# Performance work log

Hardware: AMD Instinct MI355X
Metric: run time of the kernel (lower is better)

Reference implementation:

```python
import jax, jax.numpy as jnp
import numpy as np

EPS = 1e-5
COMMITMENT_WEIGHT = 1.0


def setup_inputs() -> dict:
    key = jax.random.key(0)
    k1, k2 = jax.random.split(key)
    x = jax.random.normal(k1, (4, 4096, 128), dtype=jnp.float32)
    codebook = jax.random.normal(k2, (8192, 128), dtype=jnp.float32)
    return {"x": x, "codebook": codebook}


def _layernorm(x):
    # LayerNorm over last dim, elementwise_affine=False, eps=1e-5
    mu = jnp.mean(x, axis=-1, keepdims=True)
    var = jnp.mean(jnp.square(x - mu), axis=-1, keepdims=True)
    return (x - mu) * jax.lax.rsqrt(var + EPS)


def reference(x, codebook):
    b, n, d = x.shape
    xn = _layernorm(x)                      # [b, n, d]
    flat = xn.reshape(b * n, d)             # [bn, d]
    x2 = jnp.sum(flat * flat, axis=-1, keepdims=True)          # [bn, 1]
    e2 = jnp.sum(codebook * codebook, axis=-1)                  # [K]
    dots = jnp.einsum('nd,kd->nk', flat, codebook)              # [bn, K]
    distances = x2 - 2.0 * dots + e2[None, :]                   # [bn, K]
    embed_ind = jnp.argmin(distances, axis=-1)                  # [bn]
    quantize = codebook[embed_ind].reshape(b, n, d)             # gather
    embed_ind = embed_ind.reshape(b, n)
    loss = jnp.mean(jnp.square(quantize - xn)) * COMMITMENT_WEIGHT
    # straight-through
    quantize_st = xn + jax.lax.stop_gradient(quantize - xn)
    return (quantize_st, embed_ind, loss)
```

## Files before the change

kernel.cpp:

```cpp
#include <hip/hip_runtime.h>
#include <hip/hip_fp16.h>
#include <math.h>

typedef _Float16 half8  __attribute__((ext_vector_type(8)));
typedef _Float16 half2v __attribute__((ext_vector_type(2)));
typedef float   floatx4 __attribute__((ext_vector_type(4)));

#define ROWS   16384
#define DIM    128
#define KCODES 8192
#define NSPLIT 16
#define MTILE  512
#define NT     64
#define NCHUNK ((KCODES / NSPLIT) / NT)

__device__ __forceinline__ void async_copy16(const _Float16* src, _Float16* dst_lds) {
  __builtin_amdgcn_global_load_lds((const __attribute__((address_space(1))) void*)src,
                                   (__attribute__((address_space(3))) void*)dst_lds,
                                   16, 0, 0);
}

__global__ __launch_bounds__(256) void prep_codebook(
    const float* __restrict__ cb, _Float16* __restrict__ ehg,
    _Float16* __restrict__ elg, float* __restrict__ e2g)
{
  int tid = threadIdx.x;
  int L = tid & 63;
  int row = blockIdx.x * 4 + (tid >> 6);
  const float2* cr = (const float2*)(cb + (size_t)row * DIM);
  float2 v = cr[L];
  float s2 = v.x * v.x + v.y * v.y;
  #pragma unroll
  for (int m = 1; m < 64; m <<= 1) s2 += __shfl_xor(s2, m);
  if (L == 0) e2g[row] = -0.5f * s2;
  _Float16 h0 = (_Float16)v.x, h1 = (_Float16)v.y;
  half2v hi = {h0, h1};
  half2v lo = {(_Float16)(v.x - (float)h0), (_Float16)(v.y - (float)h1)};
  ((half2v*)(ehg + (size_t)row * DIM))[L] = hi;
  ((half2v*)(elg + (size_t)row * DIM))[L] = lo;
}

__global__ __launch_bounds__(512, 1) void argmin_kernel(
    const float* __restrict__ x, const _Float16* __restrict__ ehg,
    const _Float16* __restrict__ elg, const float* __restrict__ e2g,
    float* __restrict__ best_part, int* __restrict__ idx_part)
{
  __shared__ _Float16 ebuf[2][2][64][128];

  int tid = threadIdx.x;
  int w   = tid >> 6;
  int L   = tid & 63;
  int c   = L & 15;
  int q   = L >> 4;

  int bx = blockIdx.x;
  int mt = bx & (ROWS / MTILE - 1);
  int ns = bx >> 5;

  int rowbase = mt * MTILE + w * 64;

  half8 ah[4][4], al[4][4];

  #pragma unroll
  for (int g = 0; g < 4; ++g) {
    const float* xr = x + (size_t)(rowbase + g * 16 + c) * DIM;
    float v[32];
    #pragma unroll
    for (int ks = 0; ks < 4; ++ks) {
      float4 p0 = *(const float4*)(xr + ks * 32 + q * 8);
      float4 p1 = *(const float4*)(xr + ks * 32 + q * 8 + 4);
      v[ks*8+0] = p0.x; v[ks*8+1] = p0.y; v[ks*8+2] = p0.z; v[ks*8+3] = p0.w;
      v[ks*8+4] = p1.x; v[ks*8+5] = p1.y; v[ks*8+6] = p1.z; v[ks*8+7] = p1.w;
    }
    float s = 0.f;
    #pragma unroll
    for (int i = 0; i < 32; ++i) s += v[i];
    s += __shfl_xor(s, 16); s += __shfl_xor(s, 32);
    float mu = s * (1.0f / 128.0f);
    float s2 = 0.f;
    #pragma unroll
    for (int i = 0; i < 32; ++i) { float d = v[i] - mu; s2 += d * d; }
    s2 += __shfl_xor(s2, 16); s2 += __shfl_xor(s2, 32);
    float rstd = 1.0f / sqrtf(s2 * (1.0f / 128.0f) + 1e-5f);
    #pragma unroll
    for (int ks = 0; ks < 4; ++ks)
      #pragma unroll
      for (int j = 0; j < 8; ++j) {
        float xv = (v[ks*8+j] - mu) * rstd;
        _Float16 h = (_Float16)xv;
        ah[g][ks][j] = h;
        al[g][ks][j] = (_Float16)(xv - (float)h);
      }
  }

  float best[4][4]; int bidx[4][4];
  #pragma unroll
  for (int g = 0; g < 4; ++g)
    #pragma unroll
    for (int r = 0; r < 4; ++r) { best[g][r] = -3.4e38f; bidx[g][r] = 0; }

  int code0 = ns * (KCODES / NSPLIT);
  _Float16* lbase = &ebuf[0][0][0][0];

  auto stage = [&](int ch, int p) {
    int cbase = code0 + ch * NT;
    _Float16* lb = lbase + (size_t)p * 2 * 64 * 128;
    #pragma unroll
    for (int it = 0; it < 4; ++it) {
      int cid = it * 512 + tid;
      int arr = cid >> 10;
      int lc  = cid & 1023;
      int n   = lc >> 4;
      int kcs = lc & 15;
      int kc  = kcs ^ (n & 7);
      const _Float16* g = (arr ? elg : ehg) + (size_t)(cbase + n) * DIM + kc * 8;
      async_copy16(g, lb + (size_t)cid * 8);
    }
  };

  stage(0, 0);
  __syncthreads();

  for (int ch = 0; ch < NCHUNK; ++ch) {
    int p = ch & 1;
    int cbase = code0 + ch * NT;
    if (ch + 1 < NCHUNK) stage(ch + 1, p ^ 1);

    float e2h[4];
    #pragma unroll
    for (int s = 0; s < 4; ++s) e2h[s] = e2g[cbase + s * 16 + c];

    #pragma unroll
    for (int s = 0; s < 4; ++s) {
      int n = s * 16 + c;
      half8 bh[4], bl[4];
      #pragma unroll
      for (int ks = 0; ks < 4; ++ks) {
        int slot = ((ks * 4 + q) ^ (c & 7)) * 8;
        bh[ks] = *(const half8*)&ebuf[p][0][n][slot];
        bl[ks] = *(const half8*)&ebuf[p][1][n][slot];
      }
      int nn = cbase + n;
      #pragma unroll
      for (int g = 0; g < 4; ++g) {
        floatx4 acc = {e2h[s], e2h[s], e2h[s], e2h[s]};
        #pragma unroll
        for (int ks = 0; ks < 4; ++ks) {
          acc = __builtin_amdgcn_mfma_f32_16x16x32_f16(ah[g][ks], bh[ks], acc, 0, 0, 0);
          acc = __builtin_amdgcn_mfma_f32_16x16x32_f16(ah[g][ks], bl[ks], acc, 0, 0, 0);
          acc = __builtin_amdgcn_mfma_f32_16x16x32_f16(al[g][ks], bh[ks], acc, 0, 0, 0);
        }
        #pragma unroll
        for (int r = 0; r < 4; ++r) {
          float t = acc[r];
          if (t > best[g][r]) { best[g][r] = t; bidx[g][r] = nn; }
        }
      }
    }
    __syncthreads();
  }

  #pragma unroll
  for (int m = 1; m < 16; m <<= 1)
    #pragma unroll
    for (int g = 0; g < 4; ++g)
      #pragma unroll
      for (int r = 0; r < 4; ++r) {
        float ob = __shfl_xor(best[g][r], m);
        int   oi = __shfl_xor(bidx[g][r], m);
        if (ob > best[g][r] || (ob == best[g][r] && oi < bidx[g][r])) {
          best[g][r] = ob; bidx[g][r] = oi;
        }
      }
  if (c == 0) {
    #pragma unroll
    for (int g = 0; g < 4; ++g)
      #pragma unroll
      for (int r = 0; r < 4; ++r) {
        int row = rowbase + g * 16 + q * 4 + r;
        best_part[(size_t)row * NSPLIT + ns] = best[g][r];
        idx_part [(size_t)row * NSPLIT + ns] = bidx[g][r];
      }
  }
}

__global__ __launch_bounds__(256) void gather_loss_kernel(
    const float* __restrict__ x, const float* __restrict__ cb,
    const float* __restrict__ best_part, const int* __restrict__ idx_part,
    float* __restrict__ out_q, float* __restrict__ out_ind,
    float* __restrict__ row_loss)
{
  int tid = threadIdx.x;
  int L = tid & 63;
  int row = blockIdx.x * 4 + (tid >> 6);

  float b  = best_part[(size_t)row * NSPLIT + (L & 15)];
  int   bi = idx_part [(size_t)row * NSPLIT + (L & 15)];
  #pragma unroll
  for (int m = 1; m < 16; m <<= 1) {
    float ob = __shfl_xor(b, m);
    int   oi = __shfl_xor(bi, m);
    if (ob > b || (ob == b && oi < bi)) { b = ob; bi = oi; }
  }

  float2 qv = ((const float2*)(cb + (size_t)bi * DIM))[L];
  float2 xv = ((const float2*)(x  + (size_t)row * DIM))[L];
  float s = xv.x + xv.y;
  #pragma unroll
  for (int m = 1; m < 64; m <<= 1) s += __shfl_xor(s, m);
  float mu = s * (1.0f / 128.0f);
  float dx = xv.x - mu, dy = xv.y - mu;
  float s2 = dx * dx + dy * dy;
  #pragma unroll
  for (int m = 1; m < 64; m <<= 1) s2 += __shfl_xor(s2, m);
  float rstd = 1.0f / sqrtf(s2 * (1.0f / 128.0f) + 1e-5f);
  float xn0 = dx * rstd, xn1 = dy * rstd;
  ((float2*)out_q)[(size_t)row * 64 + L] = qv;
  float e0 = qv.x - xn0, e1 = qv.y - xn1;
  float le = e0 * e0 + e1 * e1;
  #pragma unroll
  for (int m = 1; m < 64; m <<= 1) le += __shfl_xor(le, m);
  if (L == 0) {
    row_loss[row] = le;
    out_ind[row] = (float)bi;
  }
}

__global__ __launch_bounds__(1024) void loss_reduce_kernel(
    const float* __restrict__ row_loss, float* __restrict__ out_loss)
{
  __shared__ float sm[1024];
  int tid = threadIdx.x;
  float s = 0.f;
  for (int i = tid; i < ROWS; i += 1024) s += row_loss[i];
  sm[tid] = s; __syncthreads();
  for (int st = 512; st > 0; st >>= 1) {
    if (tid < st) sm[tid] += sm[tid + st];
    __syncthreads();
  }
  if (tid == 0) *out_loss = sm[0] * (1.0f / (float)(ROWS * DIM));
}

extern "C" void kernel_launch(void* const* d_in, const int* in_sizes, int n_in,
                              void* d_out, int out_size, void* d_ws, size_t ws_size,
                              hipStream_t stream)
{
  const float* x  = (const float*)d_in[0];
  const float* cb = (const float*)d_in[1];

  char* ws = (char*)d_ws;
  _Float16* ehg      = (_Float16*)(ws + 0);
  _Float16* elg      = (_Float16*)(ws + 2097152);
  float*    e2g      = (float*)   (ws + 4194304);
  float*    best_part= (float*)   (ws + 4227072);
  int*      idx_part = (int*)     (ws + 5275648);
  float*    row_loss = (float*)   (ws + 6324224);

  float* out_q    = (float*)d_out;
  float* out_ind  = out_q + (size_t)ROWS * DIM;
  float* out_loss = out_ind + ROWS;

  prep_codebook<<<KCODES / 4, 256, 0, stream>>>(cb, ehg, elg, e2g);
  argmin_kernel<<<(ROWS / MTILE) * NSPLIT, 512, 0, stream>>>(x, ehg, elg, e2g, best_part, idx_part);
  gather_loss_kernel<<<ROWS / 4, 256, 0, stream>>>(x, cb, best_part, idx_part, out_q, out_ind, row_loss);
  loss_reduce_kernel<<<1, 1024, 0, stream>>>(row_loss, out_loss);
}
```

Measured before the change: 170.8 us.

## Drop the low-order activation MFMA and rescore top-2 candidates exactly in fp32

The argmin kernel drops the third split-precision MFMA (activation low half times codebook high half), so it issues two MFMAs per k-step instead of three. To make up for the lower accuracy it keeps the top-2 scores per split rather than the top-1. The gather kernel then rescores all 16 candidates against the fp32 codebook and picks the exact best. NSPLIT is halved to 8, so the grid has fewer blocks and each block walks more chunks. The price is extra VALU for top-2 tracking, and 16 codebook row gathers per row in the epilogue. Correctness also now relies on the true nearest code landing in some split's top-2.

New measurement: 177.1 us. 1.04x slower.

```diff
diff --git a/kernel.cpp b/kernel.cpp
--- a/kernel.cpp
+++ b/kernel.cpp
@@ -9,10 +9,11 @@
 #define ROWS   16384
 #define DIM    128
 #define KCODES 8192
-#define NSPLIT 16
+#define NSPLIT 8
 #define MTILE  512
 #define NT     64
 #define NCHUNK ((KCODES / NSPLIT) / NT)
+#define NCAND  (2 * NSPLIT)
 
 __device__ __forceinline__ void async_copy16(const _Float16* src, _Float16* dst_lds) {
   __builtin_amdgcn_global_load_lds((const __attribute__((address_space(1))) void*)src,
@@ -43,7 +44,8 @@
 __global__ __launch_bounds__(512, 1) void argmin_kernel(
     const float* __restrict__ x, const _Float16* __restrict__ ehg,
     const _Float16* __restrict__ elg, const float* __restrict__ e2g,
-    float* __restrict__ best_part, int* __restrict__ idx_part)
+    float* __restrict__ b1p, int* __restrict__ i1p,
+    float* __restrict__ b2p, int* __restrict__ i2p)
 {
   __shared__ _Float16 ebuf[2][2][64][128];
 
@@ -59,7 +61,7 @@
 
   int rowbase = mt * MTILE + w * 64;
 
-  half8 ah[4][4], al[4][4];
+  half8 ah[4][4];
 
   #pragma unroll
   for (int g = 0; g < 4; ++g) {
@@ -85,19 +87,18 @@
     #pragma unroll
     for (int ks = 0; ks < 4; ++ks)
       #pragma unroll
-      for (int j = 0; j < 8; ++j) {
-        float xv = (v[ks*8+j] - mu) * rstd;
-        _Float16 h = (_Float16)xv;
-        ah[g][ks][j] = h;
-        al[g][ks][j] = (_Float16)(xv - (float)h);
-      }
-  }
-
-  float best[4][4]; int bidx[4][4];
+      for (int j = 0; j < 8; ++j)
+        ah[g][ks][j] = (_Float16)((v[ks*8+j] - mu) * rstd);
+  }
+
+  float b1[4][4], b2[4][4]; int i1[4][4], i2[4][4];
   #pragma unroll
   for (int g = 0; g < 4; ++g)
     #pragma unroll
-    for (int r = 0; r < 4; ++r) { best[g][r] = -3.4e38f; bidx[g][r] = 0; }
+    for (int r = 0; r < 4; ++r) {
+      b1[g][r] = -3.4e38f; b2[g][r] = -3.4e38f;
+      i1[g][r] = 0; i2[g][r] = 0;
+    }
 
   int code0 = ns * (KCODES / NSPLIT);
   _Float16* lbase = &ebuf[0][0][0][0];
@@ -148,12 +149,16 @@
         for (int ks = 0; ks < 4; ++ks) {
           acc = __builtin_amdgcn_mfma_f32_16x16x32_f16(ah[g][ks], bh[ks], acc, 0, 0, 0);
           acc = __builtin_amdgcn_mfma_f32_16x16x32_f16(ah[g][ks], bl[ks], acc, 0, 0, 0);
-          acc = __builtin_amdgcn_mfma_f32_16x16x32_f16(al[g][ks], bh[ks], acc, 0, 0, 0);
         }
         #pragma unroll
         for (int r = 0; r < 4; ++r) {
           float t = acc[r];
-          if (t > best[g][r]) { best[g][r] = t; bidx[g][r] = nn; }
+          bool gt1 = t > b1[g][r];
+          bool gt2 = t > b2[g][r];
+          b2[g][r] = gt1 ? b1[g][r] : (gt2 ? t  : b2[g][r]);
+          i2[g][r] = gt1 ? i1[g][r] : (gt2 ? nn : i2[g][r]);
+          b1[g][r] = gt1 ? t  : b1[g][r];
+          i1[g][r] = gt1 ? nn : i1[g][r];
         }
       }
     }
@@ -166,10 +171,17 @@
     for (int g = 0; g < 4; ++g)
       #pragma unroll
       for (int r = 0; r < 4; ++r) {
-        float ob = __shfl_xor(best[g][r], m);
-        int   oi = __shfl_xor(bidx[g][r], m);
-        if (ob > best[g][r] || (ob == best[g][r] && oi < bidx[g][r])) {
-          best[g][r] = ob; bidx[g][r] = oi;
+        float ob1 = __shfl_xor(b1[g][r], m); int oi1 = __shfl_xor(i1[g][r], m);
+        float ob2 = __shfl_xor(b2[g][r], m); int oi2 = __shfl_xor(i2[g][r], m);
+        if (ob1 > b1[g][r]) {
+          float nb2 = (b1[g][r] >= ob2) ? b1[g][r] : ob2;
+          int   ni2 = (b1[g][r] >= ob2) ? i1[g][r] : oi2;
+          b1[g][r] = ob1; i1[g][r] = oi1;
+          b2[g][r] = nb2; i2[g][r] = ni2;
+        } else {
+          float nb2 = (ob1 >= b2[g][r]) ? ob1 : b2[g][r];
+          int   ni2 = (ob1 >= b2[g][r]) ? oi1 : i2[g][r];
+          b2[g][r] = nb2; i2[g][r] = ni2;
         }
       }
   if (c == 0) {
@@ -178,15 +190,18 @@
       #pragma unroll
       for (int r = 0; r < 4; ++r) {
         int row = rowbase + g * 16 + q * 4 + r;
-        best_part[(size_t)row * NSPLIT + ns] = best[g][r];
-        idx_part [(size_t)row * NSPLIT + ns] = bidx[g][r];
+        b1p[(size_t)row * NSPLIT + ns] = b1[g][r];
+        i1p[(size_t)row * NSPLIT + ns] = i1[g][r];
+        b2p[(size_t)row * NSPLIT + ns] = b2[g][r];
+        i2p[(size_t)row * NSPLIT + ns] = i2[g][r];
       }
   }
 }
 
 __global__ __launch_bounds__(256) void gather_loss_kernel(
     const float* __restrict__ x, const float* __restrict__ cb,
-    const float* __restrict__ best_part, const int* __restrict__ idx_part,
+    const float* __restrict__ e2g,
+    const int* __restrict__ i1p, const int* __restrict__ i2p,
     float* __restrict__ out_q, float* __restrict__ out_ind,
     float* __restrict__ row_loss)
 {
@@ -194,17 +209,11 @@
   int L = tid & 63;
   int row = blockIdx.x * 4 + (tid >> 6);
 
-  float b  = best_part[(size_t)row * NSPLIT + (L & 15)];
-  int   bi = idx_part [(size_t)row * NSPLIT + (L & 15)];
-  #pragma unroll
-  for (int m = 1; m < 16; m <<= 1) {
-    float ob = __shfl_xor(b, m);
-    int   oi = __shfl_xor(bi, m);
-    if (ob > b || (ob == b && oi < bi)) { b = ob; bi = oi; }
-  }
-
-  float2 qv = ((const float2*)(cb + (size_t)bi * DIM))[L];
-  float2 xv = ((const float2*)(x  + (size_t)row * DIM))[L];
+  int ci = 0;
+  if (L < 8)       ci = i1p[(size_t)row * NSPLIT + L];
+  else if (L < 16) ci = i2p[(size_t)row * NSPLIT + (L - 8)];
+
+  float2 xv = ((const float2*)(x + (size_t)row * DIM))[L];
   float s = xv.x + xv.y;
   #pragma unroll
   for (int m = 1; m < 64; m <<= 1) s += __shfl_xor(s, m);
@@ -215,6 +224,30 @@
   for (int m = 1; m < 64; m <<= 1) s2 += __shfl_xor(s2, m);
   float rstd = 1.0f / sqrtf(s2 * (1.0f / 128.0f) + 1e-5f);
   float xn0 = dx * rstd, xn1 = dy * rstd;
+
+  int idxs[NCAND];
+  #pragma unroll
+  for (int k = 0; k < NCAND; ++k) idxs[k] = __shfl(ci, k);
+  float2 evs[NCAND];
+  float  e2s[NCAND];
+  #pragma unroll
+  for (int k = 0; k < NCAND; ++k) {
+    evs[k] = ((const float2*)(cb + (size_t)idxs[k] * DIM))[L];
+    e2s[k] = e2g[idxs[k]];
+  }
+
+  float bestT = -3.4e38f; int bestI = 0x7fffffff;
+  #pragma unroll
+  for (int k = 0; k < NCAND; ++k) {
+    float pp = xn0 * evs[k].x + xn1 * evs[k].y;
+    #pragma unroll
+    for (int m = 1; m < 64; m <<= 1) pp += __shfl_xor(pp, m);
+    float t = pp + e2s[k];
+    int idx = idxs[k];
+    if (t > bestT || (t == bestT && idx < bestI)) { bestT = t; bestI = idx; }
+  }
+
+  float2 qv = ((const float2*)(cb + (size_t)bestI * DIM))[L];
   ((float2*)out_q)[(size_t)row * 64 + L] = qv;
   float e0 = qv.x - xn0, e1 = qv.y - xn1;
   float le = e0 * e0 + e1 * e1;
@@ -222,7 +255,7 @@
   for (int m = 1; m < 64; m <<= 1) le += __shfl_xor(le, m);
   if (L == 0) {
     row_loss[row] = le;
-    out_ind[row] = (float)bi;
+    out_ind[row] = (float)bestI;
   }
 }
 
@@ -252,8 +285,10 @@
   _Float16* ehg      = (_Float16*)(ws + 0);
   _Float16* elg      = (_Float16*)(ws + 2097152);
   float*    e2g      = (float*)   (ws + 4194304);
-  float*    best_part= (float*)   (ws + 4227072);
-  int*      idx_part = (int*)     (ws + 5275648);
+  float*    b1p      = (float*)   (ws + 4227072);
+  int*      i1p      = (int*)     (ws + 4751360);
+  float*    b2p      = (float*)   (ws + 5275648);
+  int*      i2p      = (int*)     (ws + 5799936);
   float*    row_loss = (float*)   (ws + 6324224);
 
   float* out_q    = (float*)d_out;
@@ -261,7 +296,7 @@
   float* out_loss = out_ind + ROWS;
 
   prep_codebook<<<KCODES / 4, 256, 0, stream>>>(cb, ehg, elg, e2g);
-  argmin_kernel<<<(ROWS / MTILE) * NSPLIT, 512, 0, stream>>>(x, ehg, elg, e2g, best_part, idx_part);
-  gather_loss_kernel<<<ROWS / 4, 256, 0, stream>>>(x, cb, best_part, idx_part, out_q, out_ind, row_loss);
+  argmin_kernel<<<(ROWS / MTILE) * NSPLIT, 512, 0, stream>>>(x, ehg, elg, e2g, b1p, i1p, b2p, i2p);
+  gather_loss_kernel<<<ROWS / 4, 256, 0, stream>>>(x, cb, e2g, i1p, i2p, out_q, out_ind, row_loss);
   loss_reduce_kernel<<<1, 1024, 0, stream>>>(row_loss, out_loss);
 }
```
